# Kernel optimization log

Hardware: AMD Instinct MI355X
Metric: run time of the kernel (lower is better)

The kernel has to match this reference:

```python
import jax, jax.numpy as jnp
import numpy as np

EMBED_DIM = 1024
NUM_HEADS = 16
HEAD_DIM = EMBED_DIM // NUM_HEADS  # 64


def setup_inputs() -> dict:
    key = jax.random.key(0)
    ks = jax.random.split(key, 9)
    B, S, D, Hd = 2, 2048, EMBED_DIM, HEAD_DIM
    s_in = 1.0 / np.sqrt(D)
    s_out = 1.0 / np.sqrt(D)
    return {
        "x": jax.random.normal(ks[0], (B, S, D), dtype=jnp.float32),
        # weights stored [in, out] (transpose of torch Linear.weight)
        "wq": jax.random.uniform(ks[1], (D, D), jnp.float32, -s_in, s_in),
        "bq": jax.random.uniform(ks[2], (D,), jnp.float32, -s_in, s_in),
        "wk": jax.random.uniform(ks[3], (D, Hd), jnp.float32, -s_in, s_in),
        "bk": jax.random.uniform(ks[4], (Hd,), jnp.float32, -s_in, s_in),
        "wv": jax.random.uniform(ks[5], (D, Hd), jnp.float32, -s_in, s_in),
        "bv": jax.random.uniform(ks[6], (Hd,), jnp.float32, -s_in, s_in),
        "wo": jax.random.uniform(ks[7], (D, D), jnp.float32, -s_out, s_out),
        "bo": jax.random.uniform(ks[8], (D,), jnp.float32, -s_out, s_out),
    }


def reference(x, wq, bq, wk, bk, wv, bv, wo, bo):
    B, S, D = x.shape
    H, Hd = NUM_HEADS, HEAD_DIM
    q = (x @ wq + bq).reshape(B, S, H, Hd)  # per-head queries
    k = x @ wk + bk                          # shared single-head keys  [B,S,Hd]
    v = x @ wv + bv                          # shared single-head values [B,S,Hd]
    # NOTE: original scales by embed_dim**-0.5 (not head_dim) — keep faithful.
    scores = jnp.einsum('bqhd,bkd->bhqk', q, k) / jnp.sqrt(jnp.float32(D))
    attn = jax.nn.softmax(scores, axis=-1)
    out = jnp.einsum('bhqk,bkd->bqhd', attn, v).reshape(B, S, D)
    return out @ wo + bo
```

## Files before the change

### kernel.cpp

```cpp
#include <hip/hip_runtime.h>

typedef unsigned short ushort_t;
typedef __attribute__((ext_vector_type(8))) short short8;
typedef __attribute__((ext_vector_type(4))) float f32x4;

#define EMBED 1024
#define NHEADS 16
#define HDIM 64
#define SEQ 2048
#define BATCH 2
#define BS (BATCH*SEQ)
#define QSCALE 0.045084234f

static __device__ __forceinline__ ushort_t f2b(float x) {
    union { float f; unsigned u; } v; v.f = x;
    unsigned r = v.u + 0x7FFFu + ((v.u >> 16) & 1u);
    return (ushort_t)(r >> 16);
}

static __device__ __forceinline__ void gload_lds16(const void* g, void* l) {
    __builtin_amdgcn_global_load_lds(
        (const __attribute__((address_space(1))) void*)g,
        (__attribute__((address_space(3))) void*)l, 16, 0, 0);
}

static __device__ __forceinline__ float exp2_raw(float x) {
    float r;
    asm("v_exp_f32 %0, %1" : "=v"(r) : "v"(x));
    return r;
}

__global__ __launch_bounds__(256) void prep_kernel(
    const float* __restrict__ x,
    const float* __restrict__ wq, const float* __restrict__ wk,
    const float* __restrict__ wv, const float* __restrict__ wo,
    ushort_t* __restrict__ xb, ushort_t* __restrict__ wqkv_t,
    ushort_t* __restrict__ wo_t)
{
    __shared__ float LsT[64][65];
    const int bid = blockIdx.x;
    const int t = threadIdx.x;

    if (bid < 2048) {
        const size_t i = ((size_t)bid * 256 + t) * 8;
        float4 f0 = *reinterpret_cast<const float4*>(x + i);
        float4 f1 = *reinterpret_cast<const float4*>(x + i + 4);
        short8 h;
        h[0] = (short)f2b(f0.x); h[1] = (short)f2b(f0.y);
        h[2] = (short)f2b(f0.z); h[3] = (short)f2b(f0.w);
        h[4] = (short)f2b(f1.x); h[5] = (short)f2b(f1.y);
        h[6] = (short)f2b(f1.z); h[7] = (short)f2b(f1.w);
        *reinterpret_cast<short8*>(xb + i) = h;
        return;
    }

    const float* src; ushort_t* dst; int N, bx, by;
    if (bid < 2304)      { int r = bid - 2048; src = wq; dst = wqkv_t;            N = 1024; bx = r & 15; by = r >> 4; }
    else if (bid < 2320) { int r = bid - 2304; src = wk; dst = wqkv_t + 1024*1024; N = 64;  bx = 0;      by = r; }
    else if (bid < 2336) { int r = bid - 2320; src = wv; dst = wqkv_t + 1088*1024; N = 64;  bx = 0;      by = r; }
    else                 { int r = bid - 2336; src = wo; dst = wo_t;              N = 1024; bx = r & 15; by = r >> 4; }
    const int n0 = bx * 64, k0 = by * 64;
    const int rr0 = t >> 4;
    const int c4 = (t & 15) * 4;
    #pragma unroll
    for (int rr = 0; rr < 4; ++rr) {
        float4 f = *reinterpret_cast<const float4*>(
            src + (size_t)(k0 + rr0 + rr * 16) * N + n0 + c4);
        LsT[c4 + 0][rr0 + rr * 16] = f.x;
        LsT[c4 + 1][rr0 + rr * 16] = f.y;
        LsT[c4 + 2][rr0 + rr * 16] = f.z;
        LsT[c4 + 3][rr0 + rr * 16] = f.w;
    }
    __syncthreads();
    const int rn = t >> 2;
    const int c16 = (t & 3) * 16;
    ushort_t* d = dst + (size_t)(n0 + rn) * 1024 + k0 + c16;
    short8 h0, h1;
    #pragma unroll
    for (int i = 0; i < 8; ++i) h0[i] = (short)f2b(LsT[rn][c16 + i]);
    #pragma unroll
    for (int i = 0; i < 8; ++i) h1[i] = (short)f2b(LsT[rn][c16 + 8 + i]);
    *reinterpret_cast<short8*>(d) = h0;
    *reinterpret_cast<short8*>(d + 8) = h1;
}

template<int MODE>
__global__ __launch_bounds__(256, 3) void mfma_gemm(
    const ushort_t* __restrict__ A, const ushort_t* __restrict__ Bt,
    const float* __restrict__ b0, const float* __restrict__ b1,
    const float* __restrict__ b2,
    float* __restrict__ Of, ushort_t* __restrict__ Oq,
    ushort_t* __restrict__ Okb, ushort_t* __restrict__ Ovt)
{
    __shared__ char smem[49152];

    const int tid = threadIdx.x;
    const int lane = tid & 63;
    const int w = tid >> 6;
    const int g = lane >> 4;
    const int c = lane & 15;
    const int rowBase = blockIdx.y * 128;
    const int colBase = blockIdx.x * 64;

    const int lr = lane >> 3;
    const int so = ((lane & 7) * 16) ^ (lr << 4);

    const char* Abase = (const char*)A + (size_t)rowBase * 2048;
    const char* Bbase = (const char*)Bt + (size_t)colBase * 2048;

    f32x4 acc[2][4];
    #pragma unroll
    for (int i = 0; i < 2; ++i)
        #pragma unroll
        for (int j = 0; j < 4; ++j)
            acc[i][j] = (f32x4){0.f, 0.f, 0.f, 0.f};

    #define STAGE(step, buf) do {                                              \
        char* T_ = smem + (buf) * 24576;                                       \
        const size_t kb_ = (size_t)(step) * 128;                               \
        _Pragma("unroll")                                                      \
        for (int u = 0; u < 4; ++u) {                                          \
            const int ca = 4 * w + u;                                          \
            gload_lds16(Abase + (size_t)(ca * 8 + lr) * 2048 + kb_ + so,       \
                        T_ + ca * 1024);                                       \
        }                                                                      \
        _Pragma("unroll")                                                      \
        for (int u = 0; u < 2; ++u) {                                          \
            const int cb = 2 * w + u;                                          \
            gload_lds16(Bbase + (size_t)(cb * 8 + lr) * 2048 + kb_ + so,       \
                        T_ + 16384 + cb * 1024);                               \
        }                                                                      \
    } while (0)

    STAGE(0, 0);
    __syncthreads();

    for (int i = 0; i < 16; ++i) {
        const int cur = i & 1;
        if (i < 15) STAGE(i + 1, cur ^ 1);

        const char* As = smem + cur * 24576;
        const char* Bs = As + 16384;
        #pragma unroll
        for (int ks = 0; ks < 2; ++ks) {
            short8 af[2], bf[4];
            #pragma unroll
            for (int mt = 0; mt < 2; ++mt) {
                const int row = w * 32 + mt * 16 + c;
                af[mt] = *reinterpret_cast<const short8*>(
                    As + row * 128 + ((ks * 64 + g * 16) ^ ((row & 7) << 4)));
            }
            #pragma unroll
            for (int nt = 0; nt < 4; ++nt) {
                const int row = nt * 16 + c;
                bf[nt] = *reinterpret_cast<const short8*>(
                    Bs + row * 128 + ((ks * 64 + g * 16) ^ ((row & 7) << 4)));
            }
            #pragma unroll
            for (int mt = 0; mt < 2; ++mt)
                #pragma unroll
                for (int nt = 0; nt < 4; ++nt)
                    acc[mt][nt] = __builtin_amdgcn_mfma_f32_16x16x32_bf16(
                        af[mt], bf[nt], acc[mt][nt], 0, 0, 0);
        }

        __syncthreads();
    }
    #undef STAGE

    #pragma unroll
    for (int nt = 0; nt < 4; ++nt) {
        const int colAbs = colBase + nt * 16 + c;
        #pragma unroll
        for (int mt = 0; mt < 2; ++mt) {
            const int rowA = rowBase + w * 32 + mt * 16 + g * 4;
            #pragma unroll
            for (int r = 0; r < 4; ++r) {
                const float v = acc[mt][nt][r];
                const int row = rowA + r;
                if (MODE == 2) {
                    Of[(size_t)row * 1024 + colAbs] = v + b0[colAbs];
                } else {
                    if (colAbs < 1024) {
                        Oq[(size_t)row * 1024 + colAbs] = f2b((v + b0[colAbs]) * QSCALE);
                    } else if (colAbs < 1088) {
                        const int kc = colAbs - 1024;
                        Okb[(size_t)row * 64 + kc] = f2b(v + b1[kc]);
                    } else {
                        const int hd = colAbs - 1088;
                        const int bb = row >> 11, s = row & 2047;
                        const int key = s & 63;
                        const int pos = (key & 0x23) | ((key & 0x0C) << 1) | ((key & 0x10) >> 2);
                        Ovt[((((size_t)bb * 32 + (s >> 6)) * 4 + (hd >> 4)) * 16
                             + (hd & 15)) * 64 + pos] = f2b(v + b2[hd]);
                    }
                }
            }
        }
    }
}

#define PSWZ(row, kbyte) ((row) * 128 + ((kbyte) ^ (((row) & 7) << 4)))

__global__ __launch_bounds__(512, 4) void attn_mfma_kernel(
    const ushort_t* __restrict__ q,
    const ushort_t* __restrict__ kb,
    const ushort_t* __restrict__ vt,
    ushort_t* __restrict__ aout)
{
    __shared__ char smem[65536];
    char* Ks0 = smem;
    char* Ks1 = smem + 16384;
    char* Vs0 = smem + 32768;
    char* Vs1 = smem + 49152;

    const int tid = threadIdx.x;
    const int lane = tid & 63;
    const int w = tid >> 6;
    const int g = lane >> 4;
    const int c = lane & 15;
    const int bid = blockIdx.x;
    const int qt = bid & 31;
    const int hp = (bid >> 5) & 7;
    const int b = bid >> 8;
    const int q0 = qt * 64;
    const int h = hp * 2 + (w >> 2);
    const int wq = w & 3;

    short8 bq[2];
    {
        const size_t qrow = (size_t)(b * SEQ + q0 + wq * 16 + c) * 1024 + h * 64;
        bq[0] = *reinterpret_cast<const short8*>(q + qrow + g * 8);
        bq[1] = *reinterpret_cast<const short8*>(q + qrow + 32 + g * 8);
    }

    short8 vone;
    #pragma unroll
    for (int i = 0; i < 8; ++i) vone[i] = (short)0x3F80;

    const char* kbb = (const char*)kb + (size_t)b * SEQ * 128;
    const char* vbb = (const char*)vt + (size_t)b * 262144;

    const int lr = lane >> 3;
    const int so = ((lane & 7) * 16) ^ (lr << 4);

    f32x4 oacc[4];
    #pragma unroll
    for (int i = 0; i < 4; ++i) oacc[i] = (f32x4){0.f, 0.f, 0.f, 0.f};
    f32x4 lacc = (f32x4){0.f, 0.f, 0.f, 0.f};

    #pragma unroll
    for (int u = 0; u < 4; ++u) {
        const int ch = w * 4 + u;
        const int cc = ch & 15;
        const size_t srcoff = (size_t)(cc * 8 + lr) * 128 + so;
        if (ch < 16) gload_lds16(kbb + srcoff, Ks0 + cc * 1024);
        else         gload_lds16(vbb + srcoff, Vs0 + cc * 1024);
    }
    __syncthreads();

    const int csw = (c & 7) << 4;

    for (int kt = 0; kt < SEQ / 128; ++kt) {
        char* ksb = (kt & 1) ? Ks1 : Ks0;
        char* vsb = (kt & 1) ? Vs1 : Vs0;
        char* ksn = (kt & 1) ? Ks0 : Ks1;
        char* vsn = (kt & 1) ? Vs0 : Vs1;

        {
            const int ktn = (kt < SEQ / 128 - 1) ? kt + 1 : kt;
            const char* gKt = kbb + (size_t)ktn * 16384;
            const char* gVt = vbb + (size_t)ktn * 16384;
            #pragma unroll
            for (int u = 0; u < 4; ++u) {
                const int ch = w * 4 + u;
                const int cc = ch & 15;
                const size_t srcoff = (size_t)(cc * 8 + lr) * 128 + so;
                if (ch < 16) gload_lds16(gKt + srcoff, ksn + cc * 1024);
                else         gload_lds16(gVt + srcoff, vsn + cc * 1024);
            }
        }

        #pragma unroll
        for (int sub = 0; sub < 2; ++sub) {
            const char* ksub = ksb + sub * 8192;
            const char* vsub = vsb + sub * 8192;

            f32x4 sacc[4];
            __builtin_amdgcn_s_setprio(1);
            #pragma unroll
            for (int mt = 0; mt < 4; ++mt) {
                const char* kr = ksub + (mt * 16 + c) * 128;
                short8 k0 = *reinterpret_cast<const short8*>(kr + ((g * 16) ^ csw));
                short8 k1 = *reinterpret_cast<const short8*>(kr + ((64 + g * 16) ^ csw));
                f32x4 z = (f32x4){0.f, 0.f, 0.f, 0.f};
                z = __builtin_amdgcn_mfma_f32_16x16x32_bf16(k0, bq[0], z, 0, 0, 0);
                z = __builtin_amdgcn_mfma_f32_16x16x32_bf16(k1, bq[1], z, 0, 0, 0);
                sacc[mt] = z;
            }
            __builtin_amdgcn_s_setprio(0);

            float pe[4][4];
            #pragma unroll
            for (int mt = 0; mt < 4; ++mt)
                #pragma unroll
                for (int r = 0; r < 4; ++r)
                    pe[mt][r] = exp2_raw(sacc[mt][r]);

            union U { unsigned u[4]; short8 s8; };
            U pa[2];
            #pragma unroll
            for (int ks = 0; ks < 2; ++ks) {
                asm("v_cvt_pk_bf16_f32 %0, %1, %2" : "=v"(pa[ks].u[0])
                    : "v"(pe[2*ks][0]), "v"(pe[2*ks][1]));
                asm("v_cvt_pk_bf16_f32 %0, %1, %2" : "=v"(pa[ks].u[1])
                    : "v"(pe[2*ks][2]), "v"(pe[2*ks][3]));
                asm("v_cvt_pk_bf16_f32 %0, %1, %2" : "=v"(pa[ks].u[2])
                    : "v"(pe[2*ks+1][0]), "v"(pe[2*ks+1][1]));
                asm("v_cvt_pk_bf16_f32 %0, %1, %2" : "=v"(pa[ks].u[3])
                    : "v"(pe[2*ks+1][2]), "v"(pe[2*ks+1][3]));
            }

            #pragma unroll
            for (int ks = 0; ks < 2; ++ks) {
                __builtin_amdgcn_s_setprio(1);
                #pragma unroll
                for (int nt = 0; nt < 4; ++nt) {
                    short8 vf = *reinterpret_cast<const short8*>(
                        vsub + (nt * 16 + c) * 128 + ((ks * 64 + g * 16) ^ csw));
                    oacc[nt] = __builtin_amdgcn_mfma_f32_16x16x32_bf16(
                        pa[ks].s8, vf, oacc[nt], 0, 0, 0);
                }
                lacc = __builtin_amdgcn_mfma_f32_16x16x32_bf16(
                    pa[ks].s8, vone, lacc, 0, 0, 0);
                __builtin_amdgcn_s_setprio(0);
            }
        }

        __syncthreads();
    }

    float linv[4];
    #pragma unroll
    for (int r = 0; r < 4; ++r) linv[r] = 1.0f / lacc[r];
    char* escr = smem + (w << 11);
    #pragma unroll
    for (int nt = 0; nt < 4; ++nt)
        #pragma unroll
        for (int r = 0; r < 4; ++r)
            *reinterpret_cast<ushort_t*>(escr + PSWZ(g * 4 + r, (nt * 16 + c) * 2)) =
                f2b(oacc[nt][r] * linv[r]);
    {
        const int qr = lane >> 2, ch = lane & 3;
        uint4 d0 = *reinterpret_cast<const uint4*>(escr + PSWZ(qr, ch * 32));
        uint4 d1 = *reinterpret_cast<const uint4*>(escr + PSWZ(qr, ch * 32 + 16));
        ushort_t* dst = aout + (size_t)(b * SEQ + q0 + wq * 16 + qr) * 1024 + h * 64 + ch * 16;
        *reinterpret_cast<uint4*>(dst) = d0;
        *reinterpret_cast<uint4*>(dst + 8) = d1;
    }
}

extern "C" void kernel_launch(void* const* d_in, const int* in_sizes, int n_in,
                              void* d_out, int out_size, void* d_ws, size_t ws_size,
                              hipStream_t stream) {
    const float* x  = (const float*)d_in[0];
    const float* wq = (const float*)d_in[1];
    const float* bq = (const float*)d_in[2];
    const float* wk = (const float*)d_in[3];
    const float* bk = (const float*)d_in[4];
    const float* wv = (const float*)d_in[5];
    const float* bv = (const float*)d_in[6];
    const float* wo = (const float*)d_in[7];
    const float* bo = (const float*)d_in[8];
    float* out = (float*)d_out;

    ushort_t* ws     = (ushort_t*)d_ws;
    ushort_t* wqkv_t = ws;
    ushort_t* wo_t   = wqkv_t + 1152 * 1024;
    ushort_t* kbuf   = wo_t + 1024 * 1024;
    ushort_t* vtb    = kbuf + (size_t)BS * 64;
    ushort_t* qabuf  = vtb + (size_t)BS * 64;
    ushort_t* xb     = (ushort_t*)d_out;

    prep_kernel<<<2592, 256, 0, stream>>>(x, wq, wk, wv, wo, xb, wqkv_t, wo_t);

    mfma_gemm<0><<<dim3(18, 32), 256, 0, stream>>>(xb, wqkv_t, bq, bk, bv,
                                                   nullptr, qabuf, kbuf, vtb);
    attn_mfma_kernel<<<BATCH * (NHEADS / 2) * (SEQ / 64), 512, 0, stream>>>(
        qabuf, kbuf, vtb, qabuf);
    mfma_gemm<2><<<dim3(16, 32), 256, 0, stream>>>(qabuf, wo_t, bo, nullptr, nullptr,
                                                   out, nullptr, nullptr, nullptr);
}
```

Baseline: 88.08 us.

## Swizzle GEMM block order across XCDs and batch attention sub-tiles per iteration

```diff
diff --git a/kernel.cpp b/kernel.cpp
--- a/kernel.cpp
+++ b/kernel.cpp
@@ -84,7 +84,7 @@
     *reinterpret_cast<short8*>(d + 8) = h1;
 }
 
-template<int MODE>
+template<int MODE, int NWGX>
 __global__ __launch_bounds__(256, 3) void mfma_gemm(
     const ushort_t* __restrict__ A, const ushort_t* __restrict__ Bt,
     const float* __restrict__ b0, const float* __restrict__ b1,
@@ -99,8 +99,12 @@
     const int w = tid >> 6;
     const int g = lane >> 4;
     const int c = lane & 15;
-    const int rowBase = blockIdx.y * 128;
-    const int colBase = blockIdx.x * 64;
+
+    const int bidl = blockIdx.y * NWGX + blockIdx.x;
+    const int cpx = (NWGX * 32) >> 3;
+    const int swz = (bidl & 7) * cpx + (bidl >> 3);
+    const int rowBase = (swz / NWGX) * 128;
+    const int colBase = (swz % NWGX) * 64;
 
     const int lr = lane >> 3;
     const int so = ((lane & 7) * 16) ^ (lr << 4);
@@ -261,6 +265,8 @@
 
     const int csw = (c & 7) << 4;
 
+    union U { unsigned u[4]; short8 s8; };
+
     for (int kt = 0; kt < SEQ / 128; ++kt) {
         char* ksb = (kt & 1) ? Ks1 : Ks0;
         char* vsb = (kt & 1) ? Vs1 : Vs0;
@@ -281,61 +287,96 @@
             }
         }
 
-        #pragma unroll
-        for (int sub = 0; sub < 2; ++sub) {
-            const char* ksub = ksb + sub * 8192;
-            const char* vsub = vsb + sub * 8192;
-
-            f32x4 sacc[4];
-            __builtin_amdgcn_s_setprio(1);
-            #pragma unroll
-            for (int mt = 0; mt < 4; ++mt) {
-                const char* kr = ksub + (mt * 16 + c) * 128;
-                short8 k0 = *reinterpret_cast<const short8*>(kr + ((g * 16) ^ csw));
-                short8 k1 = *reinterpret_cast<const short8*>(kr + ((64 + g * 16) ^ csw));
-                f32x4 z = (f32x4){0.f, 0.f, 0.f, 0.f};
-                z = __builtin_amdgcn_mfma_f32_16x16x32_bf16(k0, bq[0], z, 0, 0, 0);
-                z = __builtin_amdgcn_mfma_f32_16x16x32_bf16(k1, bq[1], z, 0, 0, 0);
-                sacc[mt] = z;
-            }
-            __builtin_amdgcn_s_setprio(0);
-
+        f32x4 sacc0[4], sacc1[4];
+        __builtin_amdgcn_s_setprio(1);
+        #pragma unroll
+        for (int mt = 0; mt < 4; ++mt) {
+            const char* kr = ksb + (mt * 16 + c) * 128;
+            short8 k0 = *reinterpret_cast<const short8*>(kr + ((g * 16) ^ csw));
+            short8 k1 = *reinterpret_cast<const short8*>(kr + ((64 + g * 16) ^ csw));
+            f32x4 z = (f32x4){0.f, 0.f, 0.f, 0.f};
+            z = __builtin_amdgcn_mfma_f32_16x16x32_bf16(k0, bq[0], z, 0, 0, 0);
+            z = __builtin_amdgcn_mfma_f32_16x16x32_bf16(k1, bq[1], z, 0, 0, 0);
+            sacc0[mt] = z;
+        }
+        #pragma unroll
+        for (int mt = 0; mt < 4; ++mt) {
+            const char* kr = ksb + 8192 + (mt * 16 + c) * 128;
+            short8 k0 = *reinterpret_cast<const short8*>(kr + ((g * 16) ^ csw));
+            short8 k1 = *reinterpret_cast<const short8*>(kr + ((64 + g * 16) ^ csw));
+            f32x4 z = (f32x4){0.f, 0.f, 0.f, 0.f};
+            z = __builtin_amdgcn_mfma_f32_16x16x32_bf16(k0, bq[0], z, 0, 0, 0);
+            z = __builtin_amdgcn_mfma_f32_16x16x32_bf16(k1, bq[1], z, 0, 0, 0);
+            sacc1[mt] = z;
+        }
+        __builtin_amdgcn_s_setprio(0);
+
+        U pa0[2], pa1[2];
+        {
             float pe[4][4];
             #pragma unroll
             for (int mt = 0; mt < 4; ++mt)
                 #pragma unroll
                 for (int r = 0; r < 4; ++r)
-                    pe[mt][r] = exp2_raw(sacc[mt][r]);
-
-            union U { unsigned u[4]; short8 s8; };
-            U pa[2];
+                    pe[mt][r] = exp2_raw(sacc0[mt][r]);
             #pragma unroll
             for (int ks = 0; ks < 2; ++ks) {
-                asm("v_cvt_pk_bf16_f32 %0, %1, %2" : "=v"(pa[ks].u[0])
+                asm("v_cvt_pk_bf16_f32 %0, %1, %2" : "=v"(pa0[ks].u[0])
                     : "v"(pe[2*ks][0]), "v"(pe[2*ks][1]));
-                asm("v_cvt_pk_bf16_f32 %0, %1, %2" : "=v"(pa[ks].u[1])
+                asm("v_cvt_pk_bf16_f32 %0, %1, %2" : "=v"(pa0[ks].u[1])
                     : "v"(pe[2*ks][2]), "v"(pe[2*ks][3]));
-                asm("v_cvt_pk_bf16_f32 %0, %1, %2" : "=v"(pa[ks].u[2])
+                asm("v_cvt_pk_bf16_f32 %0, %1, %2" : "=v"(pa0[ks].u[2])
                     : "v"(pe[2*ks+1][0]), "v"(pe[2*ks+1][1]));
-                asm("v_cvt_pk_bf16_f32 %0, %1, %2" : "=v"(pa[ks].u[3])
+                asm("v_cvt_pk_bf16_f32 %0, %1, %2" : "=v"(pa0[ks].u[3])
                     : "v"(pe[2*ks+1][2]), "v"(pe[2*ks+1][3]));
             }
-
+        }
+        {
+            float pe[4][4];
+            #pragma unroll
+            for (int mt = 0; mt < 4; ++mt)
+                #pragma unroll
+                for (int r = 0; r < 4; ++r)
+                    pe[mt][r] = exp2_raw(sacc1[mt][r]);
             #pragma unroll
             for (int ks = 0; ks < 2; ++ks) {
-                __builtin_amdgcn_s_setprio(1);
-                #pragma unroll
-                for (int nt = 0; nt < 4; ++nt) {
-                    short8 vf = *reinterpret_cast<const short8*>(
-                        vsub + (nt * 16 + c) * 128 + ((ks * 64 + g * 16) ^ csw));
-                    oacc[nt] = __builtin_amdgcn_mfma_f32_16x16x32_bf16(
-                        pa[ks].s8, vf, oacc[nt], 0, 0, 0);
-                }
-                lacc = __builtin_amdgcn_mfma_f32_16x16x32_bf16(
-                    pa[ks].s8, vone, lacc, 0, 0, 0);
-                __builtin_amdgcn_s_setprio(0);
-            }
-        }
+                asm("v_cvt_pk_bf16_f32 %0, %1, %2" : "=v"(pa1[ks].u[0])
+                    : "v"(pe[2*ks][0]), "v"(pe[2*ks][1]));
+                asm("v_cvt_pk_bf16_f32 %0, %1, %2" : "=v"(pa1[ks].u[1])
+                    : "v"(pe[2*ks][2]), "v"(pe[2*ks][3]));
+                asm("v_cvt_pk_bf16_f32 %0, %1, %2" : "=v"(pa1[ks].u[2])
+                    : "v"(pe[2*ks+1][0]), "v"(pe[2*ks+1][1]));
+                asm("v_cvt_pk_bf16_f32 %0, %1, %2" : "=v"(pa1[ks].u[3])
+                    : "v"(pe[2*ks+1][2]), "v"(pe[2*ks+1][3]));
+            }
+        }
+
+        __builtin_amdgcn_s_setprio(1);
+        #pragma unroll
+        for (int ks = 0; ks < 2; ++ks) {
+            #pragma unroll
+            for (int nt = 0; nt < 4; ++nt) {
+                short8 vf = *reinterpret_cast<const short8*>(
+                    vsb + (nt * 16 + c) * 128 + ((ks * 64 + g * 16) ^ csw));
+                oacc[nt] = __builtin_amdgcn_mfma_f32_16x16x32_bf16(
+                    pa0[ks].s8, vf, oacc[nt], 0, 0, 0);
+            }
+            lacc = __builtin_amdgcn_mfma_f32_16x16x32_bf16(
+                pa0[ks].s8, vone, lacc, 0, 0, 0);
+        }
+        #pragma unroll
+        for (int ks = 0; ks < 2; ++ks) {
+            #pragma unroll
+            for (int nt = 0; nt < 4; ++nt) {
+                short8 vf = *reinterpret_cast<const short8*>(
+                    vsb + 8192 + (nt * 16 + c) * 128 + ((ks * 64 + g * 16) ^ csw));
+                oacc[nt] = __builtin_amdgcn_mfma_f32_16x16x32_bf16(
+                    pa1[ks].s8, vf, oacc[nt], 0, 0, 0);
+            }
+            lacc = __builtin_amdgcn_mfma_f32_16x16x32_bf16(
+                pa1[ks].s8, vone, lacc, 0, 0, 0);
+        }
+        __builtin_amdgcn_s_setprio(0);
 
         __syncthreads();
     }
@@ -384,10 +425,10 @@
 
     prep_kernel<<<2592, 256, 0, stream>>>(x, wq, wk, wv, wo, xb, wqkv_t, wo_t);
 
-    mfma_gemm<0><<<dim3(18, 32), 256, 0, stream>>>(xb, wqkv_t, bq, bk, bv,
-                                                   nullptr, qabuf, kbuf, vtb);
+    mfma_gemm<0, 18><<<dim3(18, 32), 256, 0, stream>>>(xb, wqkv_t, bq, bk, bv,
+                                                       nullptr, qabuf, kbuf, vtb);
     attn_mfma_kernel<<<BATCH * (NHEADS / 2) * (SEQ / 64), 512, 0, stream>>>(
         qabuf, kbuf, vtb, qabuf);
-    mfma_gemm<2><<<dim3(16, 32), 256, 0, stream>>>(qabuf, wo_t, bo, nullptr, nullptr,
-                                                   out, nullptr, nullptr, nullptr);
-}
+    mfma_gemm<2, 16><<<dim3(16, 32), 256, 0, stream>>>(qabuf, wo_t, bo, nullptr, nullptr,
+                                                       out, nullptr, nullptr, nullptr);
+}
```

Result: faster. 85.74 us (median of 3 runs) (-2.7%).

## Software-pipeline attention QK with triple-buffered 64-key tiles and swizzle GEMM block order

Applied to the files above, without the earlier changes.

```diff
diff --git a/kernel.cpp b/kernel.cpp
--- a/kernel.cpp
+++ b/kernel.cpp
@@ -84,7 +84,7 @@
     *reinterpret_cast<short8*>(d + 8) = h1;
 }
 
-template<int MODE>
+template<int MODE, int NWGX>
 __global__ __launch_bounds__(256, 3) void mfma_gemm(
     const ushort_t* __restrict__ A, const ushort_t* __restrict__ Bt,
     const float* __restrict__ b0, const float* __restrict__ b1,
@@ -99,8 +99,12 @@
     const int w = tid >> 6;
     const int g = lane >> 4;
     const int c = lane & 15;
-    const int rowBase = blockIdx.y * 128;
-    const int colBase = blockIdx.x * 64;
+
+    const int bidl = blockIdx.y * NWGX + blockIdx.x;
+    const int cpx = (NWGX * 32) >> 3;
+    const int swz = (bidl & 7) * cpx + (bidl >> 3);
+    const int rowBase = (swz / NWGX) * 128;
+    const int colBase = (swz % NWGX) * 64;
 
     const int lr = lane >> 3;
     const int so = ((lane & 7) * 16) ^ (lr << 4);
@@ -208,11 +212,7 @@
     const ushort_t* __restrict__ vt,
     ushort_t* __restrict__ aout)
 {
-    __shared__ char smem[65536];
-    char* Ks0 = smem;
-    char* Ks1 = smem + 16384;
-    char* Vs0 = smem + 32768;
-    char* Vs1 = smem + 49152;
+    __shared__ char smem[49152];
 
     const int tid = threadIdx.x;
     const int lane = tid & 63;
@@ -243,102 +243,99 @@
 
     const int lr = lane >> 3;
     const int so = ((lane & 7) * 16) ^ (lr << 4);
+    const int csw = (c & 7) << 4;
+
+    #define STAGE64(t, dst) do {                                               \
+        _Pragma("unroll")                                                      \
+        for (int u = 0; u < 2; ++u) {                                          \
+            const int ch = w * 2 + u;                               \
+            const int cc = ch & 7;                                             \
+            const size_t srcoff = (size_t)(t) * 8192 + (cc * 8 + lr) * 128 + so; \
+            if (ch < 8) gload_lds16(kbb + srcoff, (dst) + cc * 1024);          \
+            else        gload_lds16(vbb + srcoff, (dst) + 8192 + cc * 1024);   \
+        }                                                                      \
+    } while (0)
+
+    #define QK64(buf, sacc) do {                                               \
+        _Pragma("unroll")                                                      \
+        for (int mt = 0; mt < 4; ++mt) {                                       \
+            const char* kr = (buf) + (mt * 16 + c) * 128;                      \
+            short8 k0 = *reinterpret_cast<const short8*>(kr + ((g * 16) ^ csw)); \
+            short8 k1 = *reinterpret_cast<const short8*>(kr + ((64 + g * 16) ^ csw)); \
+            f32x4 z = (f32x4){0.f, 0.f, 0.f, 0.f};                             \
+            z = __builtin_amdgcn_mfma_f32_16x16x32_bf16(k0, bq[0], z, 0, 0, 0); \
+            z = __builtin_amdgcn_mfma_f32_16x16x32_bf16(k1, bq[1], z, 0, 0, 0); \
+            (sacc)[mt] = z;                                                    \
+        }                                                                      \
+    } while (0)
 
     f32x4 oacc[4];
     #pragma unroll
     for (int i = 0; i < 4; ++i) oacc[i] = (f32x4){0.f, 0.f, 0.f, 0.f};
     f32x4 lacc = (f32x4){0.f, 0.f, 0.f, 0.f};
 
-    #pragma unroll
-    for (int u = 0; u < 4; ++u) {
-        const int ch = w * 4 + u;
-        const int cc = ch & 15;
-        const size_t srcoff = (size_t)(cc * 8 + lr) * 128 + so;
-        if (ch < 16) gload_lds16(kbb + srcoff, Ks0 + cc * 1024);
-        else         gload_lds16(vbb + srcoff, Vs0 + cc * 1024);
-    }
+    char* bA = smem;
+    char* bB = smem + 16384;
+    char* bC = smem + 32768;
+
+    STAGE64(0, bA);
+    STAGE64(1, bB);
     __syncthreads();
 
-    const int csw = (c & 7) << 4;
-
-    for (int kt = 0; kt < SEQ / 128; ++kt) {
-        char* ksb = (kt & 1) ? Ks1 : Ks0;
-        char* vsb = (kt & 1) ? Vs1 : Vs0;
-        char* ksn = (kt & 1) ? Ks0 : Ks1;
-        char* vsn = (kt & 1) ? Vs0 : Vs1;
-
-        {
-            const int ktn = (kt < SEQ / 128 - 1) ? kt + 1 : kt;
-            const char* gKt = kbb + (size_t)ktn * 16384;
-            const char* gVt = vbb + (size_t)ktn * 16384;
-            #pragma unroll
-            for (int u = 0; u < 4; ++u) {
-                const int ch = w * 4 + u;
-                const int cc = ch & 15;
-                const size_t srcoff = (size_t)(cc * 8 + lr) * 128 + so;
-                if (ch < 16) gload_lds16(gKt + srcoff, ksn + cc * 1024);
-                else         gload_lds16(gVt + srcoff, vsn + cc * 1024);
+    f32x4 sacc_c[4];
+    QK64(bA, sacc_c);
+
+    union U { unsigned u[4]; short8 s8; };
+
+    for (int kt = 0; kt < 32; ++kt) {
+        const int ktc = (kt + 2 < 32) ? kt + 2 : 31;
+        STAGE64(ktc, bC);
+
+        f32x4 sacc_n[4];
+        QK64(bB, sacc_n);
+
+        float pe[4][4];
+        #pragma unroll
+        for (int mt = 0; mt < 4; ++mt)
+            #pragma unroll
+            for (int r = 0; r < 4; ++r)
+                pe[mt][r] = exp2_raw(sacc_c[mt][r]);
+
+        U pa[2];
+        #pragma unroll
+        for (int ks = 0; ks < 2; ++ks) {
+            asm("v_cvt_pk_bf16_f32 %0, %1, %2" : "=v"(pa[ks].u[0])
+                : "v"(pe[2*ks][0]), "v"(pe[2*ks][1]));
+            asm("v_cvt_pk_bf16_f32 %0, %1, %2" : "=v"(pa[ks].u[1])
+                : "v"(pe[2*ks][2]), "v"(pe[2*ks][3]));
+            asm("v_cvt_pk_bf16_f32 %0, %1, %2" : "=v"(pa[ks].u[2])
+                : "v"(pe[2*ks+1][0]), "v"(pe[2*ks+1][1]));
+            asm("v_cvt_pk_bf16_f32 %0, %1, %2" : "=v"(pa[ks].u[3])
+                : "v"(pe[2*ks+1][2]), "v"(pe[2*ks+1][3]));
+        }
+
+        const char* vA = bA + 8192;
+        #pragma unroll
+        for (int ks = 0; ks < 2; ++ks) {
+            #pragma unroll
+            for (int nt = 0; nt < 4; ++nt) {
+                short8 vf = *reinterpret_cast<const short8*>(
+                    vA + (nt * 16 + c) * 128 + ((ks * 64 + g * 16) ^ csw));
+                oacc[nt] = __builtin_amdgcn_mfma_f32_16x16x32_bf16(
+                    pa[ks].s8, vf, oacc[nt], 0, 0, 0);
             }
+            lacc = __builtin_amdgcn_mfma_f32_16x16x32_bf16(
+                pa[ks].s8, vone, lacc, 0, 0, 0);
         }
 
-        #pragma unroll
-        for (int sub = 0; sub < 2; ++sub) {
-            const char* ksub = ksb + sub * 8192;
-            const char* vsub = vsb + sub * 8192;
-
-            f32x4 sacc[4];
-            __builtin_amdgcn_s_setprio(1);
-            #pragma unroll
-            for (int mt = 0; mt < 4; ++mt) {
-                const char* kr = ksub + (mt * 16 + c) * 128;
-                short8 k0 = *reinterpret_cast<const short8*>(kr + ((g * 16) ^ csw));
-                short8 k1 = *reinterpret_cast<const short8*>(kr + ((64 + g * 16) ^ csw));
-                f32x4 z = (f32x4){0.f, 0.f, 0.f, 0.f};
-                z = __builtin_amdgcn_mfma_f32_16x16x32_bf16(k0, bq[0], z, 0, 0, 0);
-                z = __builtin_amdgcn_mfma_f32_16x16x32_bf16(k1, bq[1], z, 0, 0, 0);
-                sacc[mt] = z;
-            }
-            __builtin_amdgcn_s_setprio(0);
-
-            float pe[4][4];
-            #pragma unroll
-            for (int mt = 0; mt < 4; ++mt)
-                #pragma unroll
-                for (int r = 0; r < 4; ++r)
-                    pe[mt][r] = exp2_raw(sacc[mt][r]);
-
-            union U { unsigned u[4]; short8 s8; };
-            U pa[2];
-            #pragma unroll
-            for (int ks = 0; ks < 2; ++ks) {
-                asm("v_cvt_pk_bf16_f32 %0, %1, %2" : "=v"(pa[ks].u[0])
-                    : "v"(pe[2*ks][0]), "v"(pe[2*ks][1]));
-                asm("v_cvt_pk_bf16_f32 %0, %1, %2" : "=v"(pa[ks].u[1])
-                    : "v"(pe[2*ks][2]), "v"(pe[2*ks][3]));
-                asm("v_cvt_pk_bf16_f32 %0, %1, %2" : "=v"(pa[ks].u[2])
-                    : "v"(pe[2*ks+1][0]), "v"(pe[2*ks+1][1]));
-                asm("v_cvt_pk_bf16_f32 %0, %1, %2" : "=v"(pa[ks].u[3])
-                    : "v"(pe[2*ks+1][2]), "v"(pe[2*ks+1][3]));
-            }
-
-            #pragma unroll
-            for (int ks = 0; ks < 2; ++ks) {
-                __builtin_amdgcn_s_setprio(1);
-                #pragma unroll
-                for (int nt = 0; nt < 4; ++nt) {
-                    short8 vf = *reinterpret_cast<const short8*>(
-                        vsub + (nt * 16 + c) * 128 + ((ks * 64 + g * 16) ^ csw));
-                    oacc[nt] = __builtin_amdgcn_mfma_f32_16x16x32_bf16(
-                        pa[ks].s8, vf, oacc[nt], 0, 0, 0);
-                }
-                lacc = __builtin_amdgcn_mfma_f32_16x16x32_bf16(
-                    pa[ks].s8, vone, lacc, 0, 0, 0);
-                __builtin_amdgcn_s_setprio(0);
-            }
-        }
-
         __syncthreads();
-    }
+
+        char* t0 = bA; bA = bB; bB = bC; bC = t0;
+        #pragma unroll
+        for (int i = 0; i < 4; ++i) sacc_c[i] = sacc_n[i];
+    }
+    #undef STAGE64
+    #undef QK64
 
     float linv[4];
     #pragma unroll
@@ -384,10 +381,10 @@
 
     prep_kernel<<<2592, 256, 0, stream>>>(x, wq, wk, wv, wo, xb, wqkv_t, wo_t);
 
-    mfma_gemm<0><<<dim3(18, 32), 256, 0, stream>>>(xb, wqkv_t, bq, bk, bv,
-                                                   nullptr, qabuf, kbuf, vtb);
+    mfma_gemm<0, 18><<<dim3(18, 32), 256, 0, stream>>>(xb, wqkv_t, bq, bk, bv,
+                                                       nullptr, qabuf, kbuf, vtb);
     attn_mfma_kernel<<<BATCH * (NHEADS / 2) * (SEQ / 64), 512, 0, stream>>>(
         qabuf, kbuf, vtb, qabuf);
-    mfma_gemm<2><<<dim3(16, 32), 256, 0, stream>>>(qabuf, wo_t, bo, nullptr, nullptr,
-                                                   out, nullptr, nullptr, nullptr);
-}
+    mfma_gemm<2, 16><<<dim3(16, 32), 256, 0, stream>>>(qabuf, wo_t, bo, nullptr, nullptr,
+                                                       out, nullptr, nullptr, nullptr);
+}
```

Result: no change. 89.26 us (+1.3%).
